# Kernel optimization log

Measured on AMD Instinct MI355X. Metric: run time of the kernel, lower is better.

Reference implementation:

```python
import jax, jax.numpy as jnp
import numpy as np

# Forest topology: nodes are ordered by topological level (roots first, leaves last).
# Every node at level l>0 has exactly one parent edge to a node at level l-1.
LEVEL_SIZES = [500, 2000, 6000, 12000, 16000, 16000]
NOFF = np.cumsum([0] + LEVEL_SIZES).tolist()  # node offsets per level, len D+1
N_NODES = NOFF[-1]                            # 52500
N_LEVELS = len(LEVEL_SIZES)
X_SIZE, H_SIZE, N_MAT = 128, 64, 32


def setup_inputs() -> dict:
    rng = np.random.default_rng(0)
    x = rng.standard_normal((N_NODES, X_SIZE)).astype(np.float32)
    srcs, dsts, mids = [], [], []
    for l in range(1, N_LEVELS):
        n_l = LEVEL_SIZES[l]
        srcs.append(np.arange(NOFF[l], NOFF[l + 1], dtype=np.int64))
        dsts.append(rng.integers(NOFF[l - 1], NOFF[l], size=n_l).astype(np.int64))
        mids.append(rng.integers(0, N_MAT, size=n_l).astype(np.int64))
    edge_src = np.concatenate(srcs)   # child node ids, grouped by level
    edge_dst = np.concatenate(dsts)   # parent node ids (one level up)
    matrix_id = np.concatenate(mids)  # per-edge weight-matrix id
    sx = 1.0 / np.sqrt(X_SIZE)
    sh = 1.0 / np.sqrt(H_SIZE)
    W_iou = (rng.standard_normal((3 * H_SIZE, X_SIZE)) * sx).astype(np.float32)
    b_iou = np.zeros((1, 3 * H_SIZE), np.float32)
    W_f = (rng.standard_normal((H_SIZE, X_SIZE)) * sx).astype(np.float32)
    b_f = np.zeros((1, H_SIZE), np.float32)
    U_iou = (rng.standard_normal((N_MAT, H_SIZE, 3 * H_SIZE)) * sh).astype(np.float32)
    U_f = (rng.standard_normal((N_MAT, H_SIZE, H_SIZE)) * sh).astype(np.float32)
    return {
        'x': jnp.asarray(x), 'edge_src': jnp.asarray(edge_src),
        'edge_dst': jnp.asarray(edge_dst), 'matrix_id': jnp.asarray(matrix_id),
        'W_iou': jnp.asarray(W_iou), 'b_iou': jnp.asarray(b_iou),
        'W_f': jnp.asarray(W_f), 'b_f': jnp.asarray(b_f),
        'U_iou': jnp.asarray(U_iou), 'U_f': jnp.asarray(U_f),
    }


def reference(x, edge_src, edge_dst, matrix_id, W_iou, b_iou, W_f, b_f, U_iou, U_f):
    N = x.shape[0]
    H = U_f.shape[-1]
    # _init_matrices
    x_iou = x @ W_iou.T + b_iou          # [N, 3H]
    x_f = x @ W_f.T + b_f                # [N, H]
    h = jnp.zeros((N, H), x.dtype)
    c = jnp.zeros((N, H), x.dtype)
    Uh_sum = jnp.zeros((N, 3 * H), x.dtype)
    fc_sum = jnp.zeros((N, H), x.dtype)
    e_base = NOFF[1]  # edges are stored for nodes NOFF[1]..N, grouped by src level
    # prop_nodes_topo: leaves -> roots
    for l in range(N_LEVELS - 1, -1, -1):
        s0, s1 = NOFF[l], NOFF[l + 1]
        # apply_node_func for nodes at level l
        iou = x_iou[s0:s1] + Uh_sum[s0:s1]
        i, o, u = jnp.split(iou, 3, axis=1)
        c_l = jax.nn.sigmoid(i) * jnp.tanh(u) + fc_sum[s0:s1]
        h_l = jax.nn.sigmoid(o) * jnp.tanh(c_l)
        h = h.at[s0:s1].set(h_l)
        c = c.at[s0:s1].set(c_l)
        if l > 0:
            # message_func along edges src@level l -> dst@level l-1
            e0, e1 = s0 - e_base, s1 - e_base
            src = edge_src[e0:e1] - s0          # local index into h_l
            dst = edge_dst[e0:e1]
            mid = matrix_id[e0:e1]
            hs = h_l[src]                        # [E_l, H]
            Uh = jnp.einsum('eh,ehk->ek', hs, U_iou[mid])   # per-edge bmm [E_l, 3H]
            hf = jnp.einsum('eh,ehk->ek', hs, U_f[mid])     # [E_l, H]
            f = jax.nn.sigmoid(x_f[dst] + hf)
            fc = c_l[src] * f
            # reduce_func: scatter-sum into parents (level l-1)
            p0, p1 = NOFF[l - 1], NOFF[l]
            Uh_sum = Uh_sum.at[p0:p1].add(jax.ops.segment_sum(Uh, dst - p0, num_segments=p1 - p0))
            fc_sum = fc_sum.at[p0:p1].add(jax.ops.segment_sum(fc, dst - p0, num_segments=p1 - p0))
    return h, c
```

## Files before the change

kernel.cpp:

```cpp
#include <hip/hip_runtime.h>

#define NN 52500
#define NP 36500
#define E0 500
#define NEDGE 52000
#define NBINS 160
#define MAXEL 16000
#define NSB 143

__device__ __forceinline__ float sigmoidf_(float x) { return 1.f / (1.f + __expf(-x)); }
__device__ __forceinline__ float tanhf_(float x) {
    float e = __expf(-2.f * fabsf(x));
    return copysignf((1.f - e) / (1.f + e), x);
}

typedef __attribute__((ext_vector_type(8))) short bf16x8;
typedef __attribute__((ext_vector_type(4))) float f32x4;

__device__ __forceinline__ unsigned short f2bf_rne(float f) {
    unsigned int u = __float_as_uint(f);
    u += 0x7FFF + ((u >> 16) & 1);
    return (unsigned short)(u >> 16);
}

__device__ __forceinline__ void load_split(const float* p, bf16x8& hi, bf16x8& lo) {
    float4 a = *(const float4*)p;
    float4 b = *(const float4*)(p + 4);
    float v[8] = {a.x, a.y, a.z, a.w, b.x, b.y, b.z, b.w};
#pragma unroll
    for (int j = 0; j < 8; ++j) {
        unsigned short hu = f2bf_rne(v[j]);
        float hf = __uint_as_float((unsigned int)hu << 16);
        hi[j] = (short)hu;
        lo[j] = (short)f2bf_rne(v[j] - hf);
    }
}

__global__ __launch_bounds__(256) void zero_kernel(float* __restrict__ p, int n4) {
    int i = blockIdx.x * 256 + threadIdx.x;
    if (i < n4) ((float4*)p)[i] = (float4){0.f, 0.f, 0.f, 0.f};
}

__device__ __forceinline__ void wpack8_body(int p8,
                                            const float* __restrict__ Wiou,
                                            const float* __restrict__ Wf,
                                            unsigned short* __restrict__ Wpk) {
    if (p8 >= 4096) return;
    int p0 = p8 * 8;
    int f = p0 >> 9, lane = (p0 >> 3) & 63;
    int l15 = lane & 15, quad = lane >> 4;
    const float* src;
    unsigned short *dh, *dl;
    if (f < 48) {
        int ct = f >> 2, kt = f & 3;
        src = Wiou + (size_t)(ct * 16 + l15) * 128 + kt * 32 + quad * 8;
        dh = Wpk + f * 512 + lane * 8;
        dl = Wpk + 24576 + f * 512 + lane * 8;
    } else {
        int ff = f - 48;
        int ct = ff >> 2, kt = ff & 3;
        src = Wf + (size_t)(ct * 16 + l15) * 128 + kt * 32 + quad * 8;
        dh = Wpk + 49152 + ff * 512 + lane * 8;
        dl = Wpk + 57344 + ff * 512 + lane * 8;
    }
    bf16x8 hv, lv;
#pragma unroll
    for (int j = 0; j < 8; ++j) {
        float v = src[j];
        unsigned short hu = f2bf_rne(v);
        float hf = __uint_as_float((unsigned int)hu << 16);
        hv[j] = (short)hu;
        lv[j] = (short)f2bf_rne(v - hf);
    }
    *(bf16x8*)dh = hv;
    *(bf16x8*)dl = lv;
}

__global__ __launch_bounds__(256) void histpack_kernel(
    const int* __restrict__ edge_dst, const int* __restrict__ mat_id,
    int* __restrict__ cnt, int* __restrict__ bincnt ,
    const float* __restrict__ Uiou, const float* __restrict__ Ufm,
    const float* __restrict__ Wiou, const float* __restrict__ Wf,
    unsigned short* __restrict__ Upack, unsigned short* __restrict__ Wpk)
{
    __shared__ float sbuf[16384];
    int b = blockIdx.x;
    if (b < 204) {
        int* lb = (int*)sbuf;
        for (int i = threadIdx.x; i < NBINS; i += 256) lb[i] = 0;
        __syncthreads();
        int e = b * 256 + threadIdx.x;
        if (e < NEDGE) {
            atomicAdd(&cnt[edge_dst[e]], 1);
            int L = (e >= 2000) + (e >= 8000) + (e >= 20000) + (e >= 36000);
            atomicAdd(&lb[L * 32 + mat_id[e]], 1);
        }
        __syncthreads();
        for (int i = threadIdx.x; i < NBINS; i += 256) {
            int v = lb[i];
            if (v) atomicAdd(&bincnt[i * 16], v);
        }
    } else if (b < 236) {
        int mid = b - 204;
        const float4* s0 = (const float4*)(Uiou + (size_t)mid * 12288);
        const float4* s1 = (const float4*)(Ufm + (size_t)mid * 4096);
        float4* d4 = (float4*)sbuf;
        for (int i = threadIdx.x; i < 4096; i += 256)
            d4[i] = (i < 3072) ? s0[i] : s1[i - 3072];
        __syncthreads();
        unsigned short* dhi = Upack + (size_t)mid * 32768;
        unsigned short* dlo = dhi + 16384;
        for (int p0 = threadIdx.x * 8; p0 < 16384; p0 += 2048) {
            int f = p0 >> 9;
            int lane = (p0 >> 3) & 63;
            int kt = f & 1, ct = f >> 1;
            int kbase = kt * 32 + (lane >> 4) * 8;
            int col = ct * 16 + (lane & 15);
            bf16x8 hv, lv;
#pragma unroll
            for (int j = 0; j < 8; ++j) {
                int k = kbase + j;
                float v = (col < 192) ? sbuf[k * 192 + col]
                                      : sbuf[12288 + k * 64 + (col - 192)];
                unsigned short hu = f2bf_rne(v);
                float hf = __uint_as_float((unsigned int)hu << 16);
                hv[j] = (short)hu;
                lv[j] = (short)f2bf_rne(v - hf);
            }
            *(bf16x8*)&dhi[p0] = hv;
            *(bf16x8*)&dlo[p0] = lv;
        }
    } else {
        wpack8_body((b - 236) * 256 + threadIdx.x, Wiou, Wf, Wpk);
    }
}

__global__ __launch_bounds__(256) void scanfused_kernel(
    int* __restrict__ cursor ,
    int* __restrict__ childOff,
    const int* __restrict__ bincnt, int* __restrict__ bin_off,
    int* __restrict__ bincur,
    unsigned long long* __restrict__ lookbk)
{
    __shared__ int s[256];
    __shared__ int sbase;
    int b = blockIdx.x, t = threadIdx.x;
    int i = b * 256 + t;
    int v = (i < NP) ? cursor[i] : 0;
    s[t] = v;
    __syncthreads();
#pragma unroll
    for (int d = 1; d < 256; d <<= 1) {
        int u = (t >= d) ? s[t - d] : 0;
        __syncthreads();
        s[t] += u;
        __syncthreads();
    }
    int excl_local = s[t] - v;
    int agg = s[255];
    if (t == 0) {
        if (b == 0) {
            atomicExch(&lookbk[0], (2ULL << 32) | (unsigned)agg);
            sbase = 0;
        } else {
            atomicExch(&lookbk[b], (1ULL << 32) | (unsigned)agg);
            int base = 0;
            int j = b - 1;
            while (j >= 0) {
                unsigned long long p = atomicAdd(&lookbk[j], 0ULL);
                unsigned st = (unsigned)(p >> 32);
                if (st == 0) continue;
                base += (int)(unsigned)(p & 0xFFFFFFFFULL);
                if (st == 2) break;
                --j;
            }
            atomicExch(&lookbk[b], (2ULL << 32) | (unsigned)(base + agg));
            sbase = base;
        }
    }
    __syncthreads();
    int base = sbase;
    if (i < NP) {
        int o = excl_local + base;
        childOff[i] = o;
        cursor[i] = o;
    }
    if (b == 0 && t == 0) childOff[NP] = NEDGE;

    if (b == 0) {
        int bv = (t < NBINS) ? bincnt[t * 16] : 0;
        __syncthreads();
        s[t] = bv;
        __syncthreads();
#pragma unroll
        for (int d = 1; d < 256; d <<= 1) {
            int u = (t >= d) ? s[t - d] : 0;
            __syncthreads();
            s[t] += u;
            __syncthreads();
        }
        if (t < NBINS) {
            int o = s[t] - bv;
            bin_off[t] = o;
            bincur[t * 16] = o;
        }
        if (t == 0) bin_off[NBINS] = NEDGE;
    }
}

__global__ __launch_bounds__(256) void fill2_kernel(const int* __restrict__ edge_dst,
                                                    const int* __restrict__ mat_id,
                                                    int* __restrict__ cursor,
                                                    int* __restrict__ childList,
                                                    int* __restrict__ bincur,
                                                    int* __restrict__ ord) {
    int e = blockIdx.x * 256 + threadIdx.x;
    if (e < NEDGE) {
        int pos = atomicAdd(&cursor[edge_dst[e]], 1);
        childList[pos] = e;
        int L = (e >= 2000) + (e >= 8000) + (e >= 20000) + (e >= 36000);
        int p2 = atomicAdd(&bincur[(L * 32 + mat_id[e]) * 16], 1);
        ord[p2] = e;
    }
}

__global__ __launch_bounds__(256) void xproj_kernel(
    const float* __restrict__ x, const unsigned short* __restrict__ Wpk,
    const float* __restrict__ biou, const float* __restrict__ bfp,
    float* __restrict__ xiou_all, float* __restrict__ xf_all)
{
    __shared__ __align__(16) unsigned short sW[16384];
    int wave = threadIdx.x >> 6, lane = threadIdx.x & 63;
    int l15 = lane & 15, quad = lane >> 4;
    int rowBase = blockIdx.x * 64 + wave * 16;

    int arow = rowBase + l15;
    if (arow >= NN) arow = NN - 1;
    const float* ap = x + (size_t)arow * 128 + quad * 8;
    bf16x8 ahi[4], alo[4];
#pragma unroll
    for (int kt = 0; kt < 4; ++kt) load_split(ap + kt * 32, ahi[kt], alo[kt]);

    f32x4 acc[16];
#pragma unroll
    for (int ct = 0; ct < 16; ++ct) acc[ct] = (f32x4){0.f, 0.f, 0.f, 0.f};

    bool doF = (rowBase < NP);

    for (int p = 0; p < 4; ++p) {
        const float4* sh = (const float4*)(Wpk + (p < 3 ? p * 8192 : 49152));
        const float4* sl = (const float4*)(Wpk + (p < 3 ? 24576 + p * 8192 : 57344));
        float4* dh = (float4*)sW;
        float4* dl = (float4*)(sW + 8192);
        __syncthreads();
        for (int i = threadIdx.x; i < 1024; i += 256) {
            dh[i] = sh[i];
            dl[i] = sl[i];
        }
        __syncthreads();
        if (p < 3) {
#pragma unroll
            for (int ct4 = 0; ct4 < 4; ++ct4) {
                int ct = p * 4 + ct4;
#pragma unroll
                for (int kt = 0; kt < 4; ++kt) {
                    int fl = ct4 * 4 + kt;
                    const bf16x8 bhi = *(const bf16x8*)&sW[fl * 512 + lane * 8];
                    const bf16x8 blo = *(const bf16x8*)&sW[8192 + fl * 512 + lane * 8];
                    acc[ct] = __builtin_amdgcn_mfma_f32_16x16x32_bf16(ahi[kt], bhi, acc[ct], 0, 0, 0);
                    acc[ct] = __builtin_amdgcn_mfma_f32_16x16x32_bf16(ahi[kt], blo, acc[ct], 0, 0, 0);
                    acc[ct] = __builtin_amdgcn_mfma_f32_16x16x32_bf16(alo[kt], bhi, acc[ct], 0, 0, 0);
                }
            }
        } else if (doF) {
#pragma unroll
            for (int g2 = 0; g2 < 4; ++g2) {
#pragma unroll
                for (int kt = 0; kt < 4; ++kt) {
                    int fl = g2 * 4 + kt;
                    const bf16x8 bhi = *(const bf16x8*)&sW[fl * 512 + lane * 8];
                    const bf16x8 blo = *(const bf16x8*)&sW[8192 + fl * 512 + lane * 8];
                    acc[12 + g2] = __builtin_amdgcn_mfma_f32_16x16x32_bf16(ahi[kt], bhi, acc[12 + g2], 0, 0, 0);
                    acc[12 + g2] = __builtin_amdgcn_mfma_f32_16x16x32_bf16(ahi[kt], blo, acc[12 + g2], 0, 0, 0);
                    acc[12 + g2] = __builtin_amdgcn_mfma_f32_16x16x32_bf16(alo[kt], bhi, acc[12 + g2], 0, 0, 0);
                }
            }
        }
    }

#pragma unroll
    for (int ct = 0; ct < 12; ++ct) {
        int j = ct * 16 + l15;
        float bj = biou[j];
#pragma unroll
        for (int r = 0; r < 4; ++r) {
            int n = rowBase + quad * 4 + r;
            if (n < NN) xiou_all[(size_t)n * 192 + j] = acc[ct][r] + bj;
        }
    }
    if (doF) {
#pragma unroll
        for (int g2 = 0; g2 < 4; ++g2) {
            int j = g2 * 16 + l15;
            float bj = bfp[j];
#pragma unroll
            for (int r = 0; r < 4; ++r) {
                int n = rowBase + quad * 4 + r;
                if (n < NP) xf_all[(size_t)n * 64 + j] = acc[12 + g2][r] + bj;
            }
        }
    }
}

__global__ __launch_bounds__(256) void cellgather_kernel(
    const float* __restrict__ xiou_all, const float* __restrict__ xf_all,
    const float* __restrict__ tmp,
    const int* __restrict__ childOff, const int* __restrict__ childList,
    float* __restrict__ h_all, float* __restrict__ c_all,
    int s0, int s1, int ebase, int gather)
{
    int wid = threadIdx.x >> 6, lane = threadIdx.x & 63;
    int n = s0 + blockIdx.x * 4 + wid;
    if (n >= s1) return;

    const float* xp = xiou_all + (size_t)n * 192;
    float iv = xp[lane];
    float ov = xp[64 + lane];
    float uv = xp[128 + lane];

    float ui = 0.f, uo = 0.f, uu = 0.f, fc = 0.f;
    if (gather) {
        float xfv = xf_all[(size_t)n * 64 + lane];
        int c0 = childOff[n], c1 = childOff[n + 1];
        for (int ci = c0; ci < c1; ++ci) {
            int e = childList[ci];
            const float* tp = tmp + (size_t)(e - ebase) * 256;
            ui += tp[lane];
            uo += tp[64 + lane];
            uu += tp[128 + lane];
            fc += sigmoidf_(xfv + tp[192 + lane]) * c_all[(size_t)(e + E0) * 64 + lane];
        }
    }
    float cc = sigmoidf_(iv + ui) * tanhf_(uv + uu) + fc;
    float hh = sigmoidf_(ov + uo) * tanhf_(cc);
    h_all[(size_t)n * 64 + lane] = hh;
    c_all[(size_t)n * 64 + lane] = cc;
}

__global__ __launch_bounds__(256) void edge_gemm_kernel(
    const float* __restrict__ h_all,
    const unsigned short* __restrict__ Upack,
    const int* __restrict__ bin_off, const int* __restrict__ ord,
    float* __restrict__ tmp, int lvl, int ebase, int nbslots)
{
    int bin = lvl * 32 + (blockIdx.x & 31);
    int bslot = blockIdx.x >> 5;
    int off = bin_off[bin];
    int cnt = bin_off[bin + 1] - off;
    int mid = bin & 31;
    const unsigned short* Uhi = Upack + (size_t)mid * 32768;
    const unsigned short* Ulo = Uhi + 16384;

    int wid = threadIdx.x >> 6, lane = threadIdx.x & 63;
    int l15 = lane & 15, quad = lane >> 4;

    for (int j0 = (bslot * 4 + wid) * 16; j0 < cnt; j0 += nbslots * 64) {
        int jc = j0 + l15; if (jc > cnt - 1) jc = cnt - 1;
        int e = ord[off + jc];
        const float* hp = h_all + (size_t)(e + E0) * 64 + quad * 8;
        bf16x8 ahi[2], alo[2];
        load_split(hp, ahi[0], alo[0]);
        load_split(hp + 32, ahi[1], alo[1]);

        f32x4 acc[16];
#pragma unroll
        for (int ct = 0; ct < 16; ++ct) acc[ct] = (f32x4){0.f, 0.f, 0.f, 0.f};

#pragma unroll
        for (int ct = 0; ct < 16; ++ct) {
#pragma unroll
            for (int kt = 0; kt < 2; ++kt) {
                int f = ct * 2 + kt;
                const bf16x8 bhi = *(const bf16x8*)&Uhi[f * 512 + lane * 8];
                const bf16x8 blo = *(const bf16x8*)&Ulo[f * 512 + lane * 8];
                acc[ct] = __builtin_amdgcn_mfma_f32_16x16x32_bf16(ahi[kt], bhi, acc[ct], 0, 0, 0);
                acc[ct] = __builtin_amdgcn_mfma_f32_16x16x32_bf16(ahi[kt], blo, acc[ct], 0, 0, 0);
                acc[ct] = __builtin_amdgcn_mfma_f32_16x16x32_bf16(alo[kt], bhi, acc[ct], 0, 0, 0);
            }
        }

#pragma unroll
        for (int r = 0; r < 4; ++r) {
            int jr = j0 + quad * 4 + r;
            if (jr < cnt) {
                int e2 = ord[off + jr];
                float* op = tmp + (size_t)(e2 - ebase) * 256 + l15;
#pragma unroll
                for (int ct = 0; ct < 16; ++ct) op[ct * 16] = acc[ct][r];
            }
        }
    }
}

extern "C" void kernel_launch(void* const* d_in, const int* in_sizes, int n_in,
                              void* d_out, int out_size, void* d_ws, size_t ws_size,
                              hipStream_t stream) {
    const float* x      = (const float*)d_in[0];
    const int* edge_dst = (const int*)d_in[2];
    const int* mat_id   = (const int*)d_in[3];
    const float* Wiou   = (const float*)d_in[4];
    const float* biou   = (const float*)d_in[5];
    const float* Wf     = (const float*)d_in[6];
    const float* bfp    = (const float*)d_in[7];
    const float* Uiou   = (const float*)d_in[8];
    const float* Ufm    = (const float*)d_in[9];

    float* xiou_all = (float*)d_ws;
    float* xf_all   = xiou_all + (size_t)NN * 192;
    unsigned short* Wpk = (unsigned short*)(xf_all + (size_t)NP * 64);
    float* tmp = (float*)(Wpk + 65536);
    unsigned short* Upack = (unsigned short*)(tmp + (size_t)MAXEL * 256);
    int* bin_off   = (int*)(Upack + (size_t)32 * 32768);
    int* ord       = bin_off + 192;
    int* childOff  = ord + NEDGE;
    int* cursor    = childOff + 36504;
    int* bincnt    = cursor + NP;
    unsigned long long* lookbk = (unsigned long long*)(bincnt + 2560);
    int* bincur    = (int*)(lookbk + 144);
    int* childList = bincur + 2560;
    size_t need  = (size_t)((char*)(childList + NEDGE) - (char*)d_ws);
    if (ws_size < need) return;

    float* out_h = (float*)d_out;
    float* out_c = out_h + (size_t)NN * 64;

    static const int noff[7] = {0, 500, 2500, 8500, 20500, 36500, 52500};

    zero_kernel<<<(9837 + 255) / 256, 256, 0, stream>>>((float*)cursor, 9837);
    histpack_kernel<<<252, 256, 0, stream>>>(edge_dst, mat_id, cursor, bincnt,
                                             Uiou, Ufm, Wiou, Wf, Upack, Wpk);
    scanfused_kernel<<<NSB, 256, 0, stream>>>(cursor, childOff, bincnt, bin_off,
                                              bincur, lookbk);
    fill2_kernel<<<(NEDGE + 255) / 256, 256, 0, stream>>>(
        edge_dst, mat_id, cursor, childList, bincur, ord);
    xproj_kernel<<<(NN + 63) / 64, 256, 0, stream>>>(x, Wpk, biou, bfp,
                                                     xiou_all, xf_all);

    for (int l = 5; l >= 0; --l) {
        int s0 = noff[l], s1 = noff[l + 1], nl = s1 - s0;
        int gather = (l != 5) ? 1 : 0;
        int gebase = gather ? (noff[l + 1] - E0) : 0;
        cellgather_kernel<<<(nl + 3) / 4, 256, 0, stream>>>(
            xiou_all, xf_all, tmp, childOff, childList,
            out_h, out_c, s0, s1, gebase, gather);
        if (l >= 1) {
            int ebase = s0 - E0;
            int nbs = (nl + 1023) >> 10;
            edge_gemm_kernel<<<32 * nbs, 256, 0, stream>>>(
                out_h, Upack, bin_off, ord, tmp, l - 1, ebase, nbs);
        }
    }
}
```

Measured before the change: 253.2 us.

## Split xproj and edge GEMM output columns across more blocks

xproj now launches four blocks per 64-row tile. Each block loads a single weight panel into shared memory and computes only its column group, where before one block looped over all four panels with syncs in between. Edge GEMM blocks are likewise split into two column halves, halving accumulator registers and doubling the block count. This raises parallelism and occupancy on a small-work pipeline, at the cost of reloading the A rows (x or h) once per column split.

```diff
diff --git a/kernel.cpp b/kernel.cpp
--- a/kernel.cpp
+++ b/kernel.cpp
@@ -230,9 +230,24 @@
     float* __restrict__ xiou_all, float* __restrict__ xf_all)
 {
     __shared__ __align__(16) unsigned short sW[16384];
+    int p = blockIdx.x & 3;
+    int rowBase0 = (blockIdx.x >> 2) * 64;
+    if (p == 3 && rowBase0 >= NP) return;
+
     int wave = threadIdx.x >> 6, lane = threadIdx.x & 63;
     int l15 = lane & 15, quad = lane >> 4;
-    int rowBase = blockIdx.x * 64 + wave * 16;
+    int rowBase = rowBase0 + wave * 16;
+
+    {
+        const float4* sh = (const float4*)(Wpk + (p < 3 ? p * 8192 : 49152));
+        const float4* sl = (const float4*)(Wpk + (p < 3 ? 24576 + p * 8192 : 57344));
+        float4* dh = (float4*)sW;
+        float4* dl = (float4*)(sW + 8192);
+        for (int i = threadIdx.x; i < 1024; i += 256) {
+            dh[i] = sh[i];
+            dl[i] = sl[i];
+        }
+    }
 
     int arow = rowBase + l15;
     if (arow >= NN) arow = NN - 1;
@@ -241,64 +256,37 @@
 #pragma unroll
     for (int kt = 0; kt < 4; ++kt) load_split(ap + kt * 32, ahi[kt], alo[kt]);
 
-    f32x4 acc[16];
-#pragma unroll
-    for (int ct = 0; ct < 16; ++ct) acc[ct] = (f32x4){0.f, 0.f, 0.f, 0.f};
-
-    bool doF = (rowBase < NP);
-
-    for (int p = 0; p < 4; ++p) {
-        const float4* sh = (const float4*)(Wpk + (p < 3 ? p * 8192 : 49152));
-        const float4* sl = (const float4*)(Wpk + (p < 3 ? 24576 + p * 8192 : 57344));
-        float4* dh = (float4*)sW;
-        float4* dl = (float4*)(sW + 8192);
-        __syncthreads();
-        for (int i = threadIdx.x; i < 1024; i += 256) {
-            dh[i] = sh[i];
-            dl[i] = sl[i];
-        }
-        __syncthreads();
-        if (p < 3) {
-#pragma unroll
-            for (int ct4 = 0; ct4 < 4; ++ct4) {
-                int ct = p * 4 + ct4;
-#pragma unroll
-                for (int kt = 0; kt < 4; ++kt) {
-                    int fl = ct4 * 4 + kt;
-                    const bf16x8 bhi = *(const bf16x8*)&sW[fl * 512 + lane * 8];
-                    const bf16x8 blo = *(const bf16x8*)&sW[8192 + fl * 512 + lane * 8];
-                    acc[ct] = __builtin_amdgcn_mfma_f32_16x16x32_bf16(ahi[kt], bhi, acc[ct], 0, 0, 0);
-                    acc[ct] = __builtin_amdgcn_mfma_f32_16x16x32_bf16(ahi[kt], blo, acc[ct], 0, 0, 0);
-                    acc[ct] = __builtin_amdgcn_mfma_f32_16x16x32_bf16(alo[kt], bhi, acc[ct], 0, 0, 0);
-                }
-            }
-        } else if (doF) {
-#pragma unroll
-            for (int g2 = 0; g2 < 4; ++g2) {
-#pragma unroll
-                for (int kt = 0; kt < 4; ++kt) {
-                    int fl = g2 * 4 + kt;
-                    const bf16x8 bhi = *(const bf16x8*)&sW[fl * 512 + lane * 8];
-                    const bf16x8 blo = *(const bf16x8*)&sW[8192 + fl * 512 + lane * 8];
-                    acc[12 + g2] = __builtin_amdgcn_mfma_f32_16x16x32_bf16(ahi[kt], bhi, acc[12 + g2], 0, 0, 0);
-                    acc[12 + g2] = __builtin_amdgcn_mfma_f32_16x16x32_bf16(ahi[kt], blo, acc[12 + g2], 0, 0, 0);
-                    acc[12 + g2] = __builtin_amdgcn_mfma_f32_16x16x32_bf16(alo[kt], bhi, acc[12 + g2], 0, 0, 0);
-                }
-            }
-        }
-    }
-
-#pragma unroll
-    for (int ct = 0; ct < 12; ++ct) {
-        int j = ct * 16 + l15;
-        float bj = biou[j];
-#pragma unroll
-        for (int r = 0; r < 4; ++r) {
-            int n = rowBase + quad * 4 + r;
-            if (n < NN) xiou_all[(size_t)n * 192 + j] = acc[ct][r] + bj;
-        }
-    }
-    if (doF) {
+    __syncthreads();
+
+    f32x4 acc[4];
+#pragma unroll
+    for (int c = 0; c < 4; ++c) acc[c] = (f32x4){0.f, 0.f, 0.f, 0.f};
+
+#pragma unroll
+    for (int ct4 = 0; ct4 < 4; ++ct4) {
+#pragma unroll
+        for (int kt = 0; kt < 4; ++kt) {
+            int fl = ct4 * 4 + kt;
+            const bf16x8 bhi = *(const bf16x8*)&sW[fl * 512 + lane * 8];
+            const bf16x8 blo = *(const bf16x8*)&sW[8192 + fl * 512 + lane * 8];
+            acc[ct4] = __builtin_amdgcn_mfma_f32_16x16x32_bf16(ahi[kt], bhi, acc[ct4], 0, 0, 0);
+            acc[ct4] = __builtin_amdgcn_mfma_f32_16x16x32_bf16(ahi[kt], blo, acc[ct4], 0, 0, 0);
+            acc[ct4] = __builtin_amdgcn_mfma_f32_16x16x32_bf16(alo[kt], bhi, acc[ct4], 0, 0, 0);
+        }
+    }
+
+    if (p < 3) {
+#pragma unroll
+        for (int ct4 = 0; ct4 < 4; ++ct4) {
+            int j = (p * 4 + ct4) * 16 + l15;
+            float bj = biou[j];
+#pragma unroll
+            for (int r = 0; r < 4; ++r) {
+                int n = rowBase + quad * 4 + r;
+                if (n < NN) xiou_all[(size_t)n * 192 + j] = acc[ct4][r] + bj;
+            }
+        }
+    } else {
 #pragma unroll
         for (int g2 = 0; g2 < 4; ++g2) {
             int j = g2 * 16 + l15;
@@ -306,7 +294,7 @@
 #pragma unroll
             for (int r = 0; r < 4; ++r) {
                 int n = rowBase + quad * 4 + r;
-                if (n < NP) xf_all[(size_t)n * 64 + j] = acc[12 + g2][r] + bj;
+                if (n < NP) xf_all[(size_t)n * 64 + j] = acc[g2][r] + bj;
             }
         }
     }
@@ -354,7 +342,8 @@
     float* __restrict__ tmp, int lvl, int ebase, int nbslots)
 {
     int bin = lvl * 32 + (blockIdx.x & 31);
-    int bslot = blockIdx.x >> 5;
+    int chalf = (blockIdx.x >> 5) & 1;
+    int bslot = blockIdx.x >> 6;
     int off = bin_off[bin];
     int cnt = bin_off[bin + 1] - off;
     int mid = bin & 31;
@@ -372,20 +361,21 @@
         load_split(hp, ahi[0], alo[0]);
         load_split(hp + 32, ahi[1], alo[1]);
 
-        f32x4 acc[16];
-#pragma unroll
-        for (int ct = 0; ct < 16; ++ct) acc[ct] = (f32x4){0.f, 0.f, 0.f, 0.f};
-
-#pragma unroll
-        for (int ct = 0; ct < 16; ++ct) {
+        f32x4 acc[8];
+#pragma unroll
+        for (int c = 0; c < 8; ++c) acc[c] = (f32x4){0.f, 0.f, 0.f, 0.f};
+
+#pragma unroll
+        for (int ctl = 0; ctl < 8; ++ctl) {
+            int ct = chalf * 8 + ctl;
 #pragma unroll
             for (int kt = 0; kt < 2; ++kt) {
                 int f = ct * 2 + kt;
                 const bf16x8 bhi = *(const bf16x8*)&Uhi[f * 512 + lane * 8];
                 const bf16x8 blo = *(const bf16x8*)&Ulo[f * 512 + lane * 8];
-                acc[ct] = __builtin_amdgcn_mfma_f32_16x16x32_bf16(ahi[kt], bhi, acc[ct], 0, 0, 0);
-                acc[ct] = __builtin_amdgcn_mfma_f32_16x16x32_bf16(ahi[kt], blo, acc[ct], 0, 0, 0);
-                acc[ct] = __builtin_amdgcn_mfma_f32_16x16x32_bf16(alo[kt], bhi, acc[ct], 0, 0, 0);
+                acc[ctl] = __builtin_amdgcn_mfma_f32_16x16x32_bf16(ahi[kt], bhi, acc[ctl], 0, 0, 0);
+                acc[ctl] = __builtin_amdgcn_mfma_f32_16x16x32_bf16(ahi[kt], blo, acc[ctl], 0, 0, 0);
+                acc[ctl] = __builtin_amdgcn_mfma_f32_16x16x32_bf16(alo[kt], bhi, acc[ctl], 0, 0, 0);
             }
         }
 
@@ -396,7 +386,7 @@
                 int e2 = ord[off + jr];
                 float* op = tmp + (size_t)(e2 - ebase) * 256 + l15;
 #pragma unroll
-                for (int ct = 0; ct < 16; ++ct) op[ct * 16] = acc[ct][r];
+                for (int ctl = 0; ctl < 8; ++ctl) op[(chalf * 8 + ctl) * 16] = acc[ctl][r];
             }
         }
     }
@@ -443,8 +433,8 @@
                                               bincur, lookbk);
     fill2_kernel<<<(NEDGE + 255) / 256, 256, 0, stream>>>(
         edge_dst, mat_id, cursor, childList, bincur, ord);
-    xproj_kernel<<<(NN + 63) / 64, 256, 0, stream>>>(x, Wpk, biou, bfp,
-                                                     xiou_all, xf_all);
+    xproj_kernel<<<((NN + 63) / 64) * 4, 256, 0, stream>>>(x, Wpk, biou, bfp,
+                                                           xiou_all, xf_all);
 
     for (int l = 5; l >= 0; --l) {
         int s0 = noff[l], s1 = noff[l + 1], nl = s1 - s0;
@@ -456,7 +446,7 @@
         if (l >= 1) {
             int ebase = s0 - E0;
             int nbs = (nl + 1023) >> 10;
-            edge_gemm_kernel<<<32 * nbs, 256, 0, stream>>>(
+            edge_gemm_kernel<<<64 * nbs, 256, 0, stream>>>(
                 out_h, Upack, bin_off, ord, tmp, l - 1, ebase, nbs);
         }
     }
```

New measurement: 253.3 us. About the same (+0.0%).
